# Kernel optimization log

Measured on AMD Instinct MI355X. Metric: run time of the kernel, lower is better.

Reference implementation:

```python
import jax, jax.numpy as jnp
import numpy as np

T, E = 8192, 1024
LAYER_DEPTH, NUM_LAYERS = 12, 24


def _init_params():
    ratio_0_to_1 = LAYER_DEPTH / (NUM_LAYERS - 1)
    ratio_1_to_almost_0 = 1.0 - LAYER_DEPTH / NUM_LAYERS
    zigzag = 0.5 * (jnp.arange(1, E + 1) % 3 - 1)
    time_first = jnp.full(E, jnp.log(0.3), dtype=jnp.float32) + zigzag.astype(jnp.float32)
    h = jnp.arange(0, E, dtype=jnp.float32)
    time_decay = (-5 + 8 * (h / (E - 1)) ** (0.7 + 1.3 * ratio_0_to_1)).astype(jnp.float32)
    xr = jnp.arange(E, dtype=jnp.float32) / E
    time_mix_k = jnp.power(xr, ratio_1_to_almost_0)
    time_mix_v = time_mix_k + 0.3 * ratio_0_to_1
    time_mix_r = jnp.power(xr, 0.5 * ratio_1_to_almost_0)
    return time_first, time_decay, time_mix_k, time_mix_v, time_mix_r


def setup_inputs() -> dict:
    key = jax.random.key(0)
    kx, kk_, kv_, kr_, ko_ = jax.random.split(key, 5)
    scale = 1.0 / np.sqrt(E)
    tf, td, tmk, tmv, tmr = _init_params()
    return {
        "x": jax.random.normal(kx, (T, E), dtype=jnp.float32),
        "sx": jnp.zeros((E,), jnp.float32),
        "aa": jnp.zeros((E,), jnp.float32),
        "bb": jnp.zeros((E,), jnp.float32),
        "pp": jnp.zeros((E,), jnp.float32),
        "time_first": tf,
        "time_decay": td,
        "time_mix_k": tmk,
        "time_mix_v": tmv,
        "time_mix_r": tmr,
        "Wk": jax.random.normal(kk_, (E, E), jnp.float32) * scale,
        "Wv": jax.random.normal(kv_, (E, E), jnp.float32) * scale,
        "Wr": jax.random.normal(kr_, (E, E), jnp.float32) * scale,
        "Wo": jax.random.normal(ko_, (E, E), jnp.float32) * scale,
    }


def reference(x, sx, aa, bb, pp, time_first, time_decay,
              time_mix_k, time_mix_v, time_mix_r, Wk, Wv, Wr, Wo):
    # token-shift: previous token (or carried state sx at t=0)  [T, E]
    sx_seq = jnp.concatenate((sx[None, :], x[:-1, :]), axis=0)
    kx = x * time_mix_k + sx_seq * (1.0 - time_mix_k)
    vx = x * time_mix_v + sx_seq * (1.0 - time_mix_v)
    rx = x * time_mix_r + sx_seq * (1.0 - time_mix_r)

    r = jax.nn.sigmoid(rx @ Wr)  # [T, E]
    k = kx @ Wk                  # [T, E]
    v = vx @ Wv                  # [T, E]
    decay = -jnp.exp(time_decay)  # [E]

    def step(state, kv):
        aa_, bb_, pp_ = state
        kk, vv = kv
        ww = time_first + kk
        p = jnp.maximum(pp_, ww)
        e1 = jnp.exp(pp_ - p)
        e2 = jnp.exp(ww - p)
        out = (e1 * aa_ + e2 * vv) / (e1 * bb_ + e2)
        ww2 = decay + pp_
        p2 = jnp.maximum(ww2, kk)
        e1b = jnp.exp(ww2 - p2)
        e2b = jnp.exp(kk - p2)
        return (e1b * aa_ + e2b * vv, e1b * bb_ + e2b, p2), out

    (aa_f, bb_f, pp_f), wkv = jax.lax.scan(step, (aa, bb, pp), (k, v))
    out = x + (r * wkv) @ Wo
    return out, x[-1, :], aa_f, bb_f, pp_f
```

## Files before the change

### kernel.cpp

```cpp
#include <hip/hip_runtime.h>
#include <cstdint>
#include <cstddef>

typedef __bf16 bf16x8 __attribute__((ext_vector_type(8)));
typedef float  f32x4  __attribute__((ext_vector_type(4)));

#define TT 8192
#define EE 1024
#define LDSK 40

__device__ __forceinline__ unsigned short f2bf(float f) {
    union { float f; unsigned int u; } v; v.f = f;
    unsigned int r = v.u + 0x7FFFu + ((v.u >> 16) & 1u);
    return (unsigned short)(r >> 16);
}
__device__ __forceinline__ float b2f(unsigned int h) {
    union { unsigned int u; float f; } v; v.u = h << 16; return v.f;
}
__device__ __forceinline__ void gload_lds16(const void* g, void* l) {
    __builtin_amdgcn_global_load_lds((__attribute__((address_space(1))) void*)g,
                                     (__attribute__((address_space(3))) void*)l, 16, 0, 0);
}

__global__ void wt_kernel(const float* __restrict__ Wk, const float* __restrict__ Wv,
                          const float* __restrict__ Wr, const float* __restrict__ Wo,
                          unsigned short* __restrict__ Tk, unsigned short* __restrict__ Tv,
                          unsigned short* __restrict__ Tr, unsigned short* __restrict__ To) {
    __shared__ float tile[32][33];
    const float* W; unsigned short* D;
    switch (blockIdx.z) {
        case 0:  W = Wk; D = Tk; break;
        case 1:  W = Wv; D = Tv; break;
        case 2:  W = Wr; D = Tr; break;
        default: W = Wo; D = To; break;
    }
    const int bx = blockIdx.x * 32, by = blockIdx.y * 32;
    const int tx = threadIdx.x, ty = threadIdx.y;
#pragma unroll
    for (int r = 0; r < 4; ++r)
        tile[ty + 8 * r][tx] = W[(size_t)(by + ty + 8 * r) * EE + bx + tx];
    __syncthreads();
#pragma unroll
    for (int r = 0; r < 4; ++r)
        D[(size_t)(bx + ty + 8 * r) * EE + by + tx] = f2bf(tile[tx][ty + 8 * r]);
}

__global__ void prep_kernel(const float* __restrict__ Wk, const float* __restrict__ Wv,
                            const float* __restrict__ Wr, const float* __restrict__ Wo,
                            unsigned short* __restrict__ Tk, unsigned short* __restrict__ Tv,
                            unsigned short* __restrict__ Tr, unsigned short* __restrict__ To,
                            const float* __restrict__ x, const float* __restrict__ sx,
                            const float* __restrict__ tmk, const float* __restrict__ tmv,
                            const float* __restrict__ tmr,
                            unsigned short* __restrict__ kxb, unsigned short* __restrict__ vxb,
                            unsigned short* __restrict__ rxb) {
    const int bid = blockIdx.x;
    if (bid < 4096) {
        __shared__ float tile[32][33];
        const int z = bid >> 10;
        const float* W; unsigned short* D;
        switch (z) {
            case 0:  W = Wk; D = Tk; break;
            case 1:  W = Wv; D = Tv; break;
            case 2:  W = Wr; D = Tr; break;
            default: W = Wo; D = To; break;
        }
        const int by = ((bid >> 5) & 31) * 32, bx = (bid & 31) * 32;
        const int tx = threadIdx.x & 31, ty = threadIdx.x >> 5;
#pragma unroll
        for (int r = 0; r < 4; ++r)
            tile[ty + 8 * r][tx] = W[(size_t)(by + ty + 8 * r) * EE + bx + tx];
        __syncthreads();
#pragma unroll
        for (int r = 0; r < 4; ++r)
            D[(size_t)(bx + ty + 8 * r) * EE + by + tx] = f2bf(tile[tx][ty + 8 * r]);
    } else {
        const int gid  = (bid - 4096) * 256 + threadIdx.x;
        const int base = gid * 4;
        const int t = base >> 10;
        const int e = base & (EE - 1);
        float4 xv = *(const float4*)(x + base);
        float4 pv = (t > 0) ? *(const float4*)(x + base - EE) : *(const float4*)(sx + e);
        float4 mk = *(const float4*)(tmk + e);
        float4 mv = *(const float4*)(tmv + e);
        float4 mr = *(const float4*)(tmr + e);
        ushort4 ko, vo, ro;
        ko.x = f2bf(fmaf(mk.x, xv.x - pv.x, pv.x));
        ko.y = f2bf(fmaf(mk.y, xv.y - pv.y, pv.y));
        ko.z = f2bf(fmaf(mk.z, xv.z - pv.z, pv.z));
        ko.w = f2bf(fmaf(mk.w, xv.w - pv.w, pv.w));
        vo.x = f2bf(fmaf(mv.x, xv.x - pv.x, pv.x));
        vo.y = f2bf(fmaf(mv.y, xv.y - pv.y, pv.y));
        vo.z = f2bf(fmaf(mv.z, xv.z - pv.z, pv.z));
        vo.w = f2bf(fmaf(mv.w, xv.w - pv.w, pv.w));
        ro.x = f2bf(fmaf(mr.x, xv.x - pv.x, pv.x));
        ro.y = f2bf(fmaf(mr.y, xv.y - pv.y, pv.y));
        ro.z = f2bf(fmaf(mr.z, xv.z - pv.z, pv.z));
        ro.w = f2bf(fmaf(mr.w, xv.w - pv.w, pv.w));
        *(ushort4*)(kxb + base) = ko;
        *(ushort4*)(vxb + base) = vo;
        *(ushort4*)(rxb + base) = ro;
    }
}

__global__ __launch_bounds__(256, 2) void gemm_kvr3_db(
        const unsigned short* __restrict__ kxb, const unsigned short* __restrict__ vxb,
        const unsigned short* __restrict__ rxb,
        const unsigned short* __restrict__ Wkt, const unsigned short* __restrict__ Wvt,
        const unsigned short* __restrict__ Wrt,
        unsigned short* __restrict__ kf, unsigned short* __restrict__ vf,
        unsigned short* __restrict__ ry) {
    __shared__ __align__(16) unsigned short As[2][256 * 32];
    __shared__ __align__(16) unsigned short Bs[2][128 * 32];
    const int z = blockIdx.z;
    const unsigned short* A  = (z == 0) ? kxb : (z == 1) ? vxb : rxb;
    const unsigned short* Bt = (z == 0) ? Wkt : (z == 1) ? Wvt : Wrt;
    unsigned short* C        = (z == 0) ? kf  : (z == 1) ? vf  : ry;

    const int tid  = threadIdx.x;
    const int wave = tid >> 6, lane = tid & 63;
    const int wm = (wave >> 1) * 128, wn = (wave & 1) * 64;
    const int l15 = lane & 15, lq = lane >> 4;
    const int lrow = lane >> 2, lcol = (lane & 3) * 8;
    const int bm = blockIdx.x * 256, bn = blockIdx.y * 128;

    f32x4 acc[8][4] = {};

#define STAGE_KVR(kt, dst) {                                                      \
    _Pragma("unroll") for (int p = 0; p < 4; ++p) {                               \
        const int r0 = p * 64 + wave * 16;                                        \
        gload_lds16(A + (size_t)(bm + r0 + lrow) * 1024 + (kt) + lcol,            \
                    &As[dst][r0 * 32]); }                                         \
    _Pragma("unroll") for (int p = 0; p < 2; ++p) {                               \
        const int r0 = p * 64 + wave * 16;                                        \
        gload_lds16(Bt + (size_t)(bn + r0 + lrow) * 1024 + (kt) + lcol,           \
                    &Bs[dst][r0 * 32]); } }

    STAGE_KVR(0, 0);
    for (int it = 0; it < 32; ++it) {
        asm volatile("s_waitcnt vmcnt(0)" ::: "memory");
        __syncthreads();
        const int cur = it & 1;
        if (it < 31) STAGE_KVR((it + 1) * 32, cur ^ 1);
        bf16x8 af[8], bfr[4];
#pragma unroll
        for (int i = 0; i < 8; ++i)
            af[i] = *(const bf16x8*)(&As[cur][(wm + i * 16 + l15) * 32 + lq * 8]);
#pragma unroll
        for (int j = 0; j < 4; ++j)
            bfr[j] = *(const bf16x8*)(&Bs[cur][(wn + j * 16 + l15) * 32 + lq * 8]);
#pragma unroll
        for (int i = 0; i < 8; ++i)
#pragma unroll
            for (int j = 0; j < 4; ++j)
                acc[i][j] = __builtin_amdgcn_mfma_f32_16x16x32_bf16(af[i], bfr[j], acc[i][j], 0, 0, 0);
    }
#undef STAGE_KVR

    const bool sig = (z == 2);
#pragma unroll
    for (int i = 0; i < 8; ++i)
#pragma unroll
        for (int j = 0; j < 4; ++j) {
            const int col = bn + wn + j * 16 + l15;
#pragma unroll
            for (int r = 0; r < 4; ++r) {
                const int row = bm + wm + i * 16 + lq * 4 + r;
                float val = acc[i][j][r];
                if (sig) val = 1.f / (1.f + __expf(-val));
                C[(size_t)row * 1024 + col] = f2bf(val);
            }
        }
}

__global__ __launch_bounds__(256, 2) void gemm_wo_db(const unsigned short* __restrict__ A,
                                                     const unsigned short* __restrict__ Bt,
                                                     const float* __restrict__ Res,
                                                     float* __restrict__ C) {
    __shared__ __align__(16) unsigned short As[2][256 * 32];
    __shared__ __align__(16) unsigned short Bs[2][128 * 32];
    const int tid  = threadIdx.x;
    const int wave = tid >> 6, lane = tid & 63;
    const int wm = (wave >> 1) * 128, wn = (wave & 1) * 64;
    const int l15 = lane & 15, lq = lane >> 4;
    const int lrow = lane >> 2, lcol = (lane & 3) * 8;
    const int bm = blockIdx.x * 256, bn = blockIdx.y * 128;

    f32x4 acc[8][4] = {};

#define STAGE_WO(kt, dst) {                                                       \
    _Pragma("unroll") for (int p = 0; p < 4; ++p) {                               \
        const int r0 = p * 64 + wave * 16;                                        \
        gload_lds16(A + (size_t)(bm + r0 + lrow) * 1024 + (kt) + lcol,            \
                    &As[dst][r0 * 32]); }                                         \
    _Pragma("unroll") for (int p = 0; p < 2; ++p) {                               \
        const int r0 = p * 64 + wave * 16;                                        \
        gload_lds16(Bt + (size_t)(bn + r0 + lrow) * 1024 + (kt) + lcol,           \
                    &Bs[dst][r0 * 32]); } }

    STAGE_WO(0, 0);
    for (int it = 0; it < 32; ++it) {
        asm volatile("s_waitcnt vmcnt(0)" ::: "memory");
        __syncthreads();
        const int cur = it & 1;
        if (it < 31) STAGE_WO((it + 1) * 32, cur ^ 1);
        bf16x8 af[8], bfr[4];
#pragma unroll
        for (int i = 0; i < 8; ++i)
            af[i] = *(const bf16x8*)(&As[cur][(wm + i * 16 + l15) * 32 + lq * 8]);
#pragma unroll
        for (int j = 0; j < 4; ++j)
            bfr[j] = *(const bf16x8*)(&Bs[cur][(wn + j * 16 + l15) * 32 + lq * 8]);
#pragma unroll
        for (int i = 0; i < 8; ++i)
#pragma unroll
            for (int j = 0; j < 4; ++j)
                acc[i][j] = __builtin_amdgcn_mfma_f32_16x16x32_bf16(af[i], bfr[j], acc[i][j], 0, 0, 0);
    }
#undef STAGE_WO

#pragma unroll
    for (int i = 0; i < 8; ++i)
#pragma unroll
        for (int j = 0; j < 4; ++j) {
            const int col = bn + wn + j * 16 + l15;
#pragma unroll
            for (int r = 0; r < 4; ++r) {
                const int row = bm + wm + i * 16 + lq * 4 + r;
                const size_t idx = (size_t)row * 1024 + col;
                C[idx] = acc[i][j][r] + Res[idx];
            }
        }
}

template <int NC>
__global__ void wkv_pass_a(const unsigned short* __restrict__ k,
                           const unsigned short* __restrict__ v,
                           const float* __restrict__ td,
                           float* __restrict__ Sa, float* __restrict__ Sb, float* __restrict__ Sp) {
    const int CL = TT / NC;
    const int gid = blockIdx.x * 256 + threadIdx.x;
    const int c = gid >> 10, e = gid & (EE - 1);
    const float w = -__expf(td[e]);
    float sa = 0.f, sb = 0.f, sp = -1e30f;
    const size_t base = (size_t)c * CL * EE + e;
    for (int i = 0; i < CL; ++i) {
        const size_t idx = base + (size_t)i * EE;
        const float kk = b2f(k[idx]), vv = b2f(v[idx]);
        const float q  = fmaf(w, (float)(CL - 1 - i), kk);
        const float p2 = fmaxf(sp, q);
        const float e1 = __expf(sp - p2), e2 = __expf(q - p2);
        sa = fmaf(e1, sa, e2 * vv);
        sb = fmaf(e1, sb, e2);
        sp = p2;
    }
    Sa[gid] = sa; Sb[gid] = sb; Sp[gid] = sp;
}

__global__ void wkv_pass_b_par(const float* __restrict__ aa, const float* __restrict__ bb,
                               const float* __restrict__ pp, const float* __restrict__ td,
                               const float* __restrict__ x,
                               const float* __restrict__ Sa, const float* __restrict__ Sb,
                               const float* __restrict__ Sp,
                               float* __restrict__ ina, float* __restrict__ inb,
                               float* __restrict__ inp, float* __restrict__ outTail) {
    const int NC = 256, CL = TT / NC;
    const int e = blockIdx.x, c = threadIdx.x;
    __shared__ float sA[256], sB[256], sP[256];
    const float w = -__expf(td[e]);

    float a = Sa[c * EE + e], b = Sb[c * EE + e], p = Sp[c * EE + e];

    for (int s = 1; s < NC; s <<= 1) {
        sA[c] = a; sB[c] = b; sP[c] = p;
        __syncthreads();
        if (c >= s) {
            const float myLen = (float)(CL * min(c + 1, s));
            const float aL = sA[c - s], bL = sB[c - s], pL = sP[c - s];
            const float pLd = pL + w * myLen;
            const float pn  = fmaxf(pLd, p);
            const float e1  = __expf(pLd - pn), e2 = __expf(p - pn);
            a = fmaf(e1, aL, e2 * a);
            b = fmaf(e1, bL, e2 * b);
            p = pn;
        }
        __syncthreads();
    }

    sA[c] = a; sB[c] = b; sP[c] = p;
    __syncthreads();

    const float a0 = aa[e], b0 = bb[e], p0 = pp[e];
    float ea, eb, ep;
    if (c == 0) { ea = a0; eb = b0; ep = p0; }
    else {
        const float aL = sA[c - 1], bL = sB[c - 1], pL = sP[c - 1];
        const float p0d = p0 + w * (float)(c * CL);
        const float pn  = fmaxf(p0d, pL);
        const float e1  = __expf(p0d - pn), e2 = __expf(pL - pn);
        ea = fmaf(e1, a0, e2 * aL);
        eb = fmaf(e1, b0, e2 * bL);
        ep = pn;
    }
    ina[e * NC + c] = ea; inb[e * NC + c] = eb; inp[e * NC + c] = ep;

    if (c == NC - 1) {
        const float p0d = p0 + w * (float)TT;
        const float pn  = fmaxf(p0d, p);
        const float e1  = __expf(p0d - pn), e2 = __expf(p - pn);
        outTail[e]          = x[(size_t)(TT - 1) * EE + e];
        outTail[EE + e]     = fmaf(e1, a0, e2 * a);
        outTail[2 * EE + e] = fmaf(e1, b0, e2 * b);
        outTail[3 * EE + e] = pn;
    }
}

template <int NC>
__global__ void wkv_pass_c(const unsigned short* __restrict__ k,
                           const unsigned short* __restrict__ v,
                           const float* __restrict__ tf, const float* __restrict__ td,
                           const float* __restrict__ ina, const float* __restrict__ inb,
                           const float* __restrict__ inp,
                           unsigned short* ry) {
    const int CL = TT / NC;
    const int gid = blockIdx.x * 256 + threadIdx.x;
    const int c = gid >> 10, e = gid & (EE - 1);
    const float w = -__expf(td[e]);
    const float u = tf[e];
    float a = ina[e * NC + c], b = inb[e * NC + c], p = inp[e * NC + c];
    const size_t base = (size_t)c * CL * EE + e;
    for (int i = 0; i < CL; ++i) {
        const size_t idx = base + (size_t)i * EE;
        const float kk = b2f(k[idx]), vv = b2f(v[idx]);
        const float rr = b2f(ry[idx]);
        const float ww = u + kk;
        const float pq = fmaxf(p, ww);
        const float e1 = __expf(p - pq), e2 = __expf(ww - pq);
        const float wkv = fmaf(e1, a, e2 * vv) / fmaf(e1, b, e2);
        ry[idx] = f2bf(rr * wkv);
        const float ww2 = w + p;
        const float p2  = fmaxf(ww2, kk);
        const float e1b = __expf(ww2 - p2), e2b = __expf(kk - p2);
        a = fmaf(e1b, a, e2b * vv);
        b = fmaf(e1b, b, e2b);
        p = p2;
    }
}

__global__ void wkv_pass_b_small(const float* __restrict__ aa, const float* __restrict__ bb,
                                 const float* __restrict__ pp, const float* __restrict__ td,
                                 const float* __restrict__ x,
                                 const float* __restrict__ Sa, const float* __restrict__ Sb,
                                 const float* __restrict__ Sp,
                                 float* __restrict__ ina, float* __restrict__ inb,
                                 float* __restrict__ inp, float* __restrict__ outTail) {
    const int NC = 128, CL = TT / NC;
    const int e = blockIdx.x * 256 + threadIdx.x;
    const float w  = -__expf(td[e]);
    const float wL = w * (float)CL;
    float a = aa[e], b = bb[e], p = pp[e];
    for (int c = 0; c < NC; ++c) {
        ina[e * NC + c] = a; inb[e * NC + c] = b; inp[e * NC + c] = p;
        const int idx = c * EE + e;
        const float sa = Sa[idx], sb = Sb[idx], sp = Sp[idx];
        const float pw = p + wL;
        const float p2 = fmaxf(pw, sp);
        const float e1 = __expf(pw - p2), e2 = __expf(sp - p2);
        a = fmaf(e1, a, e2 * sa);
        b = fmaf(e1, b, e2 * sb);
        p = p2;
    }
    outTail[e]          = x[(size_t)(TT - 1) * EE + e];
    outTail[EE + e]     = a;
    outTail[2 * EE + e] = b;
    outTail[3 * EE + e] = p;
}

__global__ __launch_bounds__(256, 4) void gemm_kvr(
        const float* __restrict__ X, const float* __restrict__ SX,
        const float* __restrict__ tmk, const float* __restrict__ tmv,
        const float* __restrict__ tmr,
        const unsigned short* __restrict__ Wkt, const unsigned short* __restrict__ Wvt,
        const unsigned short* __restrict__ Wrt,
        unsigned short* __restrict__ outK, unsigned short* __restrict__ outV,
        unsigned short* __restrict__ outR) {
    __shared__ __align__(16) unsigned short As[128 * LDSK];
    __shared__ __align__(16) unsigned short Bs[128 * LDSK];
    const int z = blockIdx.z;
    const float* TM = (z == 0) ? tmk : (z == 1) ? tmv : tmr;
    const unsigned short* Bt = (z == 0) ? Wkt : (z == 1) ? Wvt : Wrt;
    unsigned short* Cout = (z == 0) ? outK : (z == 1) ? outV : outR;

    const int tid  = threadIdx.x;
    const int wave = tid >> 6, lane = tid & 63;
    const int wm = (wave >> 1) * 64, wn = (wave & 1) * 64;
    const int l15 = lane & 15, lq = lane >> 4;
    const int bm = blockIdx.x * 128, bn = blockIdx.y * 128;

    f32x4 acc[4][4] = {};

    for (int kt = 0; kt < 1024; kt += 32) {
        __syncthreads();
#pragma unroll
        for (int p = 0; p < 2; ++p) {
            const int li  = p * 256 + tid;
            const int row = li >> 2, q = li & 3;
            const int e0  = kt + q * 8;
            {
                const int t = bm + row;
                const float* xr = X + (size_t)t * EE + e0;
                const float* pr = (t > 0) ? (X + (size_t)(t - 1) * EE + e0) : (SX + e0);
                float4 xa = *(const float4*)xr, xb = *(const float4*)(xr + 4);
                float4 pa = *(const float4*)pr, pb = *(const float4*)(pr + 4);
                float4 ma = *(const float4*)(TM + e0), mb = *(const float4*)(TM + e0 + 4);
                ushort4 lo, hi;
                lo.x = f2bf(fmaf(ma.x, xa.x - pa.x, pa.x));
                lo.y = f2bf(fmaf(ma.y, xa.y - pa.y, pa.y));
                lo.z = f2bf(fmaf(ma.z, xa.z - pa.z, pa.z));
                lo.w = f2bf(fmaf(ma.w, xa.w - pa.w, pa.w));
                hi.x = f2bf(fmaf(mb.x, xb.x - pb.x, pb.x));
                hi.y = f2bf(fmaf(mb.y, xb.y - pb.y, pb.y));
                hi.z = f2bf(fmaf(mb.z, xb.z - pb.z, pb.z));
                hi.w = f2bf(fmaf(mb.w, xb.w - pb.w, pb.w));
                *(ushort4*)(&As[row * LDSK + q * 8])     = lo;
                *(ushort4*)(&As[row * LDSK + q * 8 + 4]) = hi;
            }
            *(uint4*)(&Bs[row * LDSK + q * 8]) =
                *(const uint4*)(Bt + (size_t)(bn + row) * 1024 + e0);
        }
        __syncthreads();
        bf16x8 af[4], bfr[4];
#pragma unroll
        for (int i = 0; i < 4; ++i) {
            af[i]  = *(const bf16x8*)(&As[(wm + i * 16 + l15) * LDSK + lq * 8]);
            bfr[i] = *(const bf16x8*)(&Bs[(wn + i * 16 + l15) * LDSK + lq * 8]);
        }
#pragma unroll
        for (int i = 0; i < 4; ++i)
#pragma unroll
            for (int j = 0; j < 4; ++j)
                acc[i][j] = __builtin_amdgcn_mfma_f32_16x16x32_bf16(af[i], bfr[j], acc[i][j], 0, 0, 0);
    }

    const bool sig = (z == 2);
#pragma unroll
    for (int i = 0; i < 4; ++i)
#pragma unroll
        for (int j = 0; j < 4; ++j) {
            const int col = bn + wn + j * 16 + l15;
#pragma unroll
            for (int r = 0; r < 4; ++r) {
                const int row = bm + wm + i * 16 + lq * 4 + r;
                float val = acc[i][j][r];
                if (sig) val = 1.f / (1.f + __expf(-val));
                Cout[(size_t)row * 1024 + col] = f2bf(val);
            }
        }
}

extern "C" void kernel_launch(void* const* d_in, const int* in_sizes, int n_in,
                              void* d_out, int out_size, void* d_ws, size_t ws_size,
                              hipStream_t stream) {
    const float* x   = (const float*)d_in[0];
    const float* sx  = (const float*)d_in[1];
    const float* aa  = (const float*)d_in[2];
    const float* bb  = (const float*)d_in[3];
    const float* pp  = (const float*)d_in[4];
    const float* tf  = (const float*)d_in[5];
    const float* td  = (const float*)d_in[6];
    const float* tmk = (const float*)d_in[7];
    const float* tmv = (const float*)d_in[8];
    const float* tmr = (const float*)d_in[9];
    const float* Wk  = (const float*)d_in[10];
    const float* Wv  = (const float*)d_in[11];
    const float* Wr  = (const float*)d_in[12];
    const float* Wo  = (const float*)d_in[13];
    float* out = (float*)d_out;

    char* ws = (char*)d_ws;
    const size_t MB = 1ull << 20;

    unsigned short* Wkt = (unsigned short*)(ws + 0 * MB);
    unsigned short* Wvt = (unsigned short*)(ws + 2 * MB);
    unsigned short* Wrt = (unsigned short*)(ws + 4 * MB);
    unsigned short* Wot = (unsigned short*)(ws + 6 * MB);

    if (ws_size >= 75 * MB) {
        unsigned short* rxb = (unsigned short*)(ws + 8 * MB);
        unsigned short* kf  = (unsigned short*)(ws + 24 * MB);
        unsigned short* ry  = (unsigned short*)(ws + 40 * MB);
        unsigned short* vf  = (unsigned short*)(ws + 56 * MB);
        float* Sa  = (float*)(ws + 8 * MB);
        float* Sb  = (float*)(ws + 9 * MB);
        float* Sp  = (float*)(ws + 10 * MB);
        float* ina = (float*)(ws + 11 * MB);
        float* inb = (float*)(ws + 12 * MB);
        float* inp = (float*)(ws + 13 * MB);
        unsigned short* kxb = (unsigned short*)d_out;
        unsigned short* vxb = (unsigned short*)d_out + (size_t)TT * EE;

        prep_kernel<<<12288, 256, 0, stream>>>(Wk, Wv, Wr, Wo, Wkt, Wvt, Wrt, Wot,
                                               x, sx, tmk, tmv, tmr, kxb, vxb, rxb);
        gemm_kvr3_db<<<dim3(32, 8, 3), 256, 0, stream>>>(kxb, vxb, rxb, Wkt, Wvt, Wrt,
                                                         kf, vf, ry);
        wkv_pass_a<256><<<(256 * EE) / 256, 256, 0, stream>>>(kf, vf, td, Sa, Sb, Sp);
        wkv_pass_b_par<<<EE, 256, 0, stream>>>(aa, bb, pp, td, x, Sa, Sb, Sp,
                                               ina, inb, inp, out + (size_t)TT * EE);
        wkv_pass_c<256><<<(256 * EE) / 256, 256, 0, stream>>>(kf, vf, tf, td,
                                                              ina, inb, inp, ry);
        gemm_wo_db<<<dim3(32, 8), 256, 0, stream>>>(ry, Wot, x, out);
    } else {
        unsigned short* ry = (unsigned short*)(ws + 8 * MB);
        char* scan = ws + 24 * MB;
        const size_t QK = (size_t)128 * EE * sizeof(float);
        float* Sa  = (float*)(scan);
        float* Sb  = (float*)(scan + QK);
        float* Sp  = (float*)(scan + 2 * QK);
        float* ina = (float*)(scan + 3 * QK);
        float* inb = (float*)(scan + 4 * QK);
        float* inp = (float*)(scan + 5 * QK);
        unsigned short* kf = (unsigned short*)d_out;
        unsigned short* vf = (unsigned short*)d_out + (size_t)TT * EE;

        wt_kernel<<<dim3(32, 32, 4), dim3(32, 8), 0, stream>>>(Wk, Wv, Wr, Wo, Wkt, Wvt, Wrt, Wot);
        gemm_kvr<<<dim3(64, 8, 3), 256, 0, stream>>>(x, sx, tmk, tmv, tmr,
                                                     Wkt, Wvt, Wrt, kf, vf, ry);
        wkv_pass_a<128><<<(128 * EE) / 256, 256, 0, stream>>>(kf, vf, td, Sa, Sb, Sp);
        wkv_pass_b_small<<<4, 256, 0, stream>>>(aa, bb, pp, td, x, Sa, Sb, Sp,
                                                ina, inb, inp, out + (size_t)TT * EE);
        wkv_pass_c<128><<<(128 * EE) / 256, 256, 0, stream>>>(kf, vf, tf, td,
                                                              ina, inb, inp, ry);
        gemm_wo_db<<<dim3(32, 8), 256, 0, stream>>>(ry, Wot, x, out);
    }
}
```

Baseline: 294.0 us.

## Shrink GEMM tiles to 128x128 with BK=64, drop double buffering, raise occupancy

Both the K/V/R projection GEMM and the output GEMM move from 256x128 tiles with BK=32 double-buffered LDS to 128x128 tiles with a single-buffered BK=64 stage. Launch bounds go from 2 to 4 blocks per CU and the grid doubles. The intent is to fill more CUs and hide memory latency through occupancy instead of software prefetch, with fewer accumulator registers per thread. In exchange the loads no longer overlap compute within a block, each block has an extra barrier, and there is less operand reuse per tile.

```diff
diff --git a/kernel.cpp b/kernel.cpp
--- a/kernel.cpp
+++ b/kernel.cpp
@@ -103,15 +103,15 @@
     }
 }
 
-__global__ __launch_bounds__(256, 2) void gemm_kvr3_db(
+__global__ __launch_bounds__(256, 4) void gemm_kvr3(
         const unsigned short* __restrict__ kxb, const unsigned short* __restrict__ vxb,
         const unsigned short* __restrict__ rxb,
         const unsigned short* __restrict__ Wkt, const unsigned short* __restrict__ Wvt,
         const unsigned short* __restrict__ Wrt,
         unsigned short* __restrict__ kf, unsigned short* __restrict__ vf,
         unsigned short* __restrict__ ry) {
-    __shared__ __align__(16) unsigned short As[2][256 * 32];
-    __shared__ __align__(16) unsigned short Bs[2][128 * 32];
+    __shared__ __align__(16) unsigned short As[128 * 64];
+    __shared__ __align__(16) unsigned short Bs[128 * 64];
     const int z = blockIdx.z;
     const unsigned short* A  = (z == 0) ? kxb : (z == 1) ? vxb : rxb;
     const unsigned short* Bt = (z == 0) ? Wkt : (z == 1) ? Wvt : Wrt;
@@ -119,47 +119,41 @@
 
     const int tid  = threadIdx.x;
     const int wave = tid >> 6, lane = tid & 63;
-    const int wm = (wave >> 1) * 128, wn = (wave & 1) * 64;
+    const int wm = (wave >> 1) * 64, wn = (wave & 1) * 64;
     const int l15 = lane & 15, lq = lane >> 4;
-    const int lrow = lane >> 2, lcol = (lane & 3) * 8;
-    const int bm = blockIdx.x * 256, bn = blockIdx.y * 128;
-
-    f32x4 acc[8][4] = {};
-
-#define STAGE_KVR(kt, dst) {                                                      \
-    _Pragma("unroll") for (int p = 0; p < 4; ++p) {                               \
-        const int r0 = p * 64 + wave * 16;                                        \
-        gload_lds16(A + (size_t)(bm + r0 + lrow) * 1024 + (kt) + lcol,            \
-                    &As[dst][r0 * 32]); }                                         \
-    _Pragma("unroll") for (int p = 0; p < 2; ++p) {                               \
-        const int r0 = p * 64 + wave * 16;                                        \
-        gload_lds16(Bt + (size_t)(bn + r0 + lrow) * 1024 + (kt) + lcol,           \
-                    &Bs[dst][r0 * 32]); } }
-
-    STAGE_KVR(0, 0);
-    for (int it = 0; it < 32; ++it) {
-        asm volatile("s_waitcnt vmcnt(0)" ::: "memory");
-        __syncthreads();
-        const int cur = it & 1;
-        if (it < 31) STAGE_KVR((it + 1) * 32, cur ^ 1);
-        bf16x8 af[8], bfr[4];
-#pragma unroll
-        for (int i = 0; i < 8; ++i)
-            af[i] = *(const bf16x8*)(&As[cur][(wm + i * 16 + l15) * 32 + lq * 8]);
-#pragma unroll
-        for (int j = 0; j < 4; ++j)
-            bfr[j] = *(const bf16x8*)(&Bs[cur][(wn + j * 16 + l15) * 32 + lq * 8]);
-#pragma unroll
-        for (int i = 0; i < 8; ++i)
-#pragma unroll
-            for (int j = 0; j < 4; ++j)
-                acc[i][j] = __builtin_amdgcn_mfma_f32_16x16x32_bf16(af[i], bfr[j], acc[i][j], 0, 0, 0);
-    }
-#undef STAGE_KVR
+    const int lrow = lane >> 3, lcol = (lane & 7) * 8;
+    const int bm = blockIdx.x * 128, bn = blockIdx.y * 128;
+
+    f32x4 acc[4][4] = {};
+
+    for (int kt = 0; kt < 1024; kt += 64) {
+        __syncthreads();
+#pragma unroll
+        for (int p = 0; p < 4; ++p) {
+            const int r0 = p * 32 + wave * 8;
+            gload_lds16(A  + (size_t)(bm + r0 + lrow) * 1024 + kt + lcol, &As[r0 * 64]);
+            gload_lds16(Bt + (size_t)(bn + r0 + lrow) * 1024 + kt + lcol, &Bs[r0 * 64]);
+        }
+        __syncthreads();
+#pragma unroll
+        for (int h = 0; h < 2; ++h) {
+            bf16x8 af[4], bfr[4];
+#pragma unroll
+            for (int i = 0; i < 4; ++i) {
+                af[i]  = *(const bf16x8*)(&As[(wm + i * 16 + l15) * 64 + h * 32 + lq * 8]);
+                bfr[i] = *(const bf16x8*)(&Bs[(wn + i * 16 + l15) * 64 + h * 32 + lq * 8]);
+            }
+#pragma unroll
+            for (int i = 0; i < 4; ++i)
+#pragma unroll
+                for (int j = 0; j < 4; ++j)
+                    acc[i][j] = __builtin_amdgcn_mfma_f32_16x16x32_bf16(af[i], bfr[j], acc[i][j], 0, 0, 0);
+        }
+    }
 
     const bool sig = (z == 2);
 #pragma unroll
-    for (int i = 0; i < 8; ++i)
+    for (int i = 0; i < 4; ++i)
 #pragma unroll
         for (int j = 0; j < 4; ++j) {
             const int col = bn + wn + j * 16 + l15;
@@ -173,54 +167,48 @@
         }
 }
 
-__global__ __launch_bounds__(256, 2) void gemm_wo_db(const unsigned short* __restrict__ A,
-                                                     const unsigned short* __restrict__ Bt,
-                                                     const float* __restrict__ Res,
-                                                     float* __restrict__ C) {
-    __shared__ __align__(16) unsigned short As[2][256 * 32];
-    __shared__ __align__(16) unsigned short Bs[2][128 * 32];
+__global__ __launch_bounds__(256, 4) void gemm_wo(const unsigned short* __restrict__ A,
+                                                  const unsigned short* __restrict__ Bt,
+                                                  const float* __restrict__ Res,
+                                                  float* __restrict__ C) {
+    __shared__ __align__(16) unsigned short As[128 * 64];
+    __shared__ __align__(16) unsigned short Bs[128 * 64];
     const int tid  = threadIdx.x;
     const int wave = tid >> 6, lane = tid & 63;
-    const int wm = (wave >> 1) * 128, wn = (wave & 1) * 64;
+    const int wm = (wave >> 1) * 64, wn = (wave & 1) * 64;
     const int l15 = lane & 15, lq = lane >> 4;
-    const int lrow = lane >> 2, lcol = (lane & 3) * 8;
-    const int bm = blockIdx.x * 256, bn = blockIdx.y * 128;
-
-    f32x4 acc[8][4] = {};
-
-#define STAGE_WO(kt, dst) {                                                       \
-    _Pragma("unroll") for (int p = 0; p < 4; ++p) {                               \
-        const int r0 = p * 64 + wave * 16;                                        \
-        gload_lds16(A + (size_t)(bm + r0 + lrow) * 1024 + (kt) + lcol,            \
-                    &As[dst][r0 * 32]); }                                         \
-    _Pragma("unroll") for (int p = 0; p < 2; ++p) {                               \
-        const int r0 = p * 64 + wave * 16;                                        \
-        gload_lds16(Bt + (size_t)(bn + r0 + lrow) * 1024 + (kt) + lcol,           \
-                    &Bs[dst][r0 * 32]); } }
-
-    STAGE_WO(0, 0);
-    for (int it = 0; it < 32; ++it) {
-        asm volatile("s_waitcnt vmcnt(0)" ::: "memory");
-        __syncthreads();
-        const int cur = it & 1;
-        if (it < 31) STAGE_WO((it + 1) * 32, cur ^ 1);
-        bf16x8 af[8], bfr[4];
-#pragma unroll
-        for (int i = 0; i < 8; ++i)
-            af[i] = *(const bf16x8*)(&As[cur][(wm + i * 16 + l15) * 32 + lq * 8]);
-#pragma unroll
-        for (int j = 0; j < 4; ++j)
-            bfr[j] = *(const bf16x8*)(&Bs[cur][(wn + j * 16 + l15) * 32 + lq * 8]);
-#pragma unroll
-        for (int i = 0; i < 8; ++i)
-#pragma unroll
-            for (int j = 0; j < 4; ++j)
-                acc[i][j] = __builtin_amdgcn_mfma_f32_16x16x32_bf16(af[i], bfr[j], acc[i][j], 0, 0, 0);
-    }
-#undef STAGE_WO
-
-#pragma unroll
-    for (int i = 0; i < 8; ++i)
+    const int lrow = lane >> 3, lcol = (lane & 7) * 8;
+    const int bm = blockIdx.x * 128, bn = blockIdx.y * 128;
+
+    f32x4 acc[4][4] = {};
+
+    for (int kt = 0; kt < 1024; kt += 64) {
+        __syncthreads();
+#pragma unroll
+        for (int p = 0; p < 4; ++p) {
+            const int r0 = p * 32 + wave * 8;
+            gload_lds16(A  + (size_t)(bm + r0 + lrow) * 1024 + kt + lcol, &As[r0 * 64]);
+            gload_lds16(Bt + (size_t)(bn + r0 + lrow) * 1024 + kt + lcol, &Bs[r0 * 64]);
+        }
+        __syncthreads();
+#pragma unroll
+        for (int h = 0; h < 2; ++h) {
+            bf16x8 af[4], bfr[4];
+#pragma unroll
+            for (int i = 0; i < 4; ++i) {
+                af[i]  = *(const bf16x8*)(&As[(wm + i * 16 + l15) * 64 + h * 32 + lq * 8]);
+                bfr[i] = *(const bf16x8*)(&Bs[(wn + i * 16 + l15) * 64 + h * 32 + lq * 8]);
+            }
+#pragma unroll
+            for (int i = 0; i < 4; ++i)
+#pragma unroll
+                for (int j = 0; j < 4; ++j)
+                    acc[i][j] = __builtin_amdgcn_mfma_f32_16x16x32_bf16(af[i], bfr[j], acc[i][j], 0, 0, 0);
+        }
+    }
+
+#pragma unroll
+    for (int i = 0; i < 4; ++i)
 #pragma unroll
         for (int j = 0; j < 4; ++j) {
             const int col = bn + wn + j * 16 + l15;
@@ -501,14 +489,14 @@
 
         prep_kernel<<<12288, 256, 0, stream>>>(Wk, Wv, Wr, Wo, Wkt, Wvt, Wrt, Wot,
                                                x, sx, tmk, tmv, tmr, kxb, vxb, rxb);
-        gemm_kvr3_db<<<dim3(32, 8, 3), 256, 0, stream>>>(kxb, vxb, rxb, Wkt, Wvt, Wrt,
-                                                         kf, vf, ry);
+        gemm_kvr3<<<dim3(64, 8, 3), 256, 0, stream>>>(kxb, vxb, rxb, Wkt, Wvt, Wrt,
+                                                      kf, vf, ry);
         wkv_pass_a<256><<<(256 * EE) / 256, 256, 0, stream>>>(kf, vf, td, Sa, Sb, Sp);
         wkv_pass_b_par<<<EE, 256, 0, stream>>>(aa, bb, pp, td, x, Sa, Sb, Sp,
                                                ina, inb, inp, out + (size_t)TT * EE);
         wkv_pass_c<256><<<(256 * EE) / 256, 256, 0, stream>>>(kf, vf, tf, td,
                                                               ina, inb, inp, ry);
-        gemm_wo_db<<<dim3(32, 8), 256, 0, stream>>>(ry, Wot, x, out);
+        gemm_wo<<<dim3(64, 8), 256, 0, stream>>>(ry, Wot, x, out);
     } else {
         unsigned short* ry = (unsigned short*)(ws + 8 * MB);
         char* scan = ws + 24 * MB;
@@ -530,6 +518,6 @@
                                                 ina, inb, inp, out + (size_t)TT * EE);
         wkv_pass_c<128><<<(128 * EE) / 256, 256, 0, stream>>>(kf, vf, tf, td,
                                                               ina, inb, inp, ry);
-        gemm_wo_db<<<dim3(32, 8), 256, 0, stream>>>(ry, Wot, x, out);
-    }
-}
+        gemm_wo<<<dim3(64, 8), 256, 0, stream>>>(ry, Wot, x, out);
+    }
+}
```

Result: faster. 253.4 us (-13.8%).
